# Kernel tuning notes

Measured on AMD Instinct MI355X. Metric: run time of the kernel, lower is better.

## Reference

```python
import jax, jax.numpy as jnp
import numpy as np

HIDDEN_DIM = 2048
NUM_HEADS = 16
HEAD_DIM = HIDDEN_DIM // NUM_HEADS


def setup_inputs() -> dict:
    key = jax.random.key(0)
    ks = jax.random.split(key, 5)
    B, S, D = 1, 2048, HIDDEN_DIM
    scale = 1.0 / np.sqrt(D)
    return {
        "x": jax.random.normal(ks[0], (B, S, D), dtype=jnp.float32),
        "w_q": jax.random.normal(ks[1], (D, D), dtype=jnp.float32) * scale,
        "w_k": jax.random.normal(ks[2], (D, D), dtype=jnp.float32) * scale,
        "w_v": jax.random.normal(ks[3], (D, D), dtype=jnp.float32) * scale,
        "w_o": jax.random.normal(ks[4], (D, D), dtype=jnp.float32) * scale,
    }


def reference(x, w_q, w_k, w_v, w_o):
    # x: (B, S, D). Projections use x @ W.T as in the torch module.
    B, S, D = x.shape
    H, Hd = NUM_HEADS, HEAD_DIM
    q = (x @ w_q.T).reshape(B, S, H, Hd)
    k = (x @ w_k.T).reshape(B, S, H, Hd)
    v = (x @ w_v.T).reshape(B, S, H, Hd)
    scale = 1.0 / np.sqrt(Hd).astype(np.float32)
    # The tiled online-softmax loop computes exact softmax attention.
    scores = jnp.einsum("bqhd,bkhd->bhqk", q, k) * scale  # (B,H,S,S)
    p = jax.nn.softmax(scores, axis=-1)
    o = jnp.einsum("bhqk,bkhd->bqhd", p, v).reshape(B, S, D)
    return o @ w_o.T
```

## Files before the change

kernel.cpp:

```cpp
#include <hip/hip_runtime.h>
#include <hip/hip_bf16.h>
#include <cstdint>
#include <cstddef>

typedef __bf16 bf16x8 __attribute__((ext_vector_type(8)));
typedef float f32x4 __attribute__((ext_vector_type(4)));
typedef unsigned short u16x8 __attribute__((ext_vector_type(8)));
typedef unsigned short u16x4 __attribute__((ext_vector_type(4)));

#define S_LEN 2048
#define DMODEL 2048
#define NHEADS 16
#define HD 128

__device__ inline unsigned short f2bf(float f) {
  union { float f; unsigned int u; } v; v.f = f;
  unsigned int r = (v.u + 0x7fffu + ((v.u >> 16) & 1u)) >> 16;
  return (unsigned short)r;
}

__device__ __forceinline__ void gload16(const unsigned short* g,
                                        unsigned short* lds) {
  __builtin_amdgcn_global_load_lds(
      (const __attribute__((address_space(1))) void*)g,
      (__attribute__((address_space(3))) void*)lds, 16, 0, 0);
}

__global__ void cast_all(const float* __restrict__ x, const float* __restrict__ wq,
                         const float* __restrict__ wk, const float* __restrict__ wv,
                         const float* __restrict__ wo,
                         unsigned short* __restrict__ out, float qscale) {
  const int b = blockIdx.x;
  const int seg = b >> 12;
  const int i = ((b & 4095) * 256 + threadIdx.x) * 4;
  const float* src = seg == 0 ? x : seg == 1 ? wq : seg == 2 ? wk
                   : seg == 3 ? wv : wo;
  const float scale = (seg == 1) ? qscale : 1.0f;
  unsigned short* dst = out + (size_t)seg * ((size_t)S_LEN * DMODEL);
  float4 v = *(const float4*)(src + i);
  u16x4 o;
  o.x = f2bf(v.x * scale); o.y = f2bf(v.y * scale);
  o.z = f2bf(v.z * scale); o.w = f2bf(v.w * scale);
  *(u16x4*)(dst + i) = o;
}

template <int MODE>
__device__ __forceinline__ void gemm_core(
    const unsigned short* __restrict__ A, const unsigned short* __restrict__ B,
    float* __restrict__ Cf, unsigned short* __restrict__ Cb,
    int M, int N, int K, int m0, int n0,
    unsigned short* As, unsigned short* Bs) {
  constexpr int BK = 32;
  const int tid = threadIdx.x;
  const int wave = tid >> 6, lane = tid & 63;
  const int lg = lane >> 4, lr = lane & 15;
  const int rw = (wave >> 1) * 64;
  const int cw = (wave & 1) * 64;

  const int c0 = tid, c1 = tid + 256;
  const unsigned short* Ap0 = A + (size_t)(m0 + (c0 >> 2)) * K + (c0 & 3) * 8;
  const unsigned short* Ap1 = A + (size_t)(m0 + (c1 >> 2)) * K + (c1 & 3) * 8;
  const unsigned short* Bp0 = B + (size_t)(n0 + (c0 >> 2)) * K + (c0 & 3) * 8;
  const unsigned short* Bp1 = B + (size_t)(n0 + (c1 >> 2)) * K + (c1 & 3) * 8;
  unsigned short* as0 = As + wave * 512;
  unsigned short* as1 = As + 2048 + wave * 512;
  unsigned short* bs0 = Bs + wave * 512;
  unsigned short* bs1 = Bs + 2048 + wave * 512;

  f32x4 acc[4][4];
#pragma unroll
  for (int i = 0; i < 4; i++)
#pragma unroll
    for (int j = 0; j < 4; j++) acc[i][j] = (f32x4){0.f, 0.f, 0.f, 0.f};

  const int nk = K / BK;
  for (int kt = 0; kt < nk; ++kt) {
    const int ko = kt * BK;
    __syncthreads();
    gload16(Ap0 + ko, as0);
    gload16(Ap1 + ko, as1);
    gload16(Bp0 + ko, bs0);
    gload16(Bp1 + ko, bs1);
    __syncthreads();

    bf16x8 af[4], bfr[4];
#pragma unroll
    for (int mt = 0; mt < 4; mt++)
      af[mt] = *(const bf16x8*)(As + (rw + mt * 16 + lr) * BK + lg * 8);
#pragma unroll
    for (int nt = 0; nt < 4; nt++)
      bfr[nt] = *(const bf16x8*)(Bs + (cw + nt * 16 + lr) * BK + lg * 8);
#pragma unroll
    for (int mt = 0; mt < 4; mt++)
#pragma unroll
      for (int nt = 0; nt < 4; nt++)
        acc[mt][nt] = __builtin_amdgcn_mfma_f32_16x16x32_bf16(
            af[mt], bfr[nt], acc[mt][nt], 0, 0, 0);
  }

#pragma unroll
  for (int mt = 0; mt < 4; mt++)
#pragma unroll
    for (int nt = 0; nt < 4; nt++) {
      const int col = n0 + cw + nt * 16 + lr;
#pragma unroll
      for (int r = 0; r < 4; r++) {
        const int row = m0 + rw + mt * 16 + lg * 4 + r;
        const float v = acc[mt][nt][r];
        if (MODE == 0) Cf[(size_t)row * N + col] = v;
        else if (MODE == 1) Cb[(size_t)row * N + col] = f2bf(v);
        else Cb[(size_t)col * M + row] = f2bf(v);
      }
    }
}

template <int MODE>
__global__ __launch_bounds__(256, 2) void gemm_bt(
    const unsigned short* __restrict__ A, const unsigned short* __restrict__ B,
    float* __restrict__ Cf, unsigned short* __restrict__ Cb,
    int M, int N, int K) {
  __shared__ unsigned short As[128 * 32];
  __shared__ unsigned short Bs[128 * 32];
  gemm_core<MODE>(A, B, Cf, Cb, M, N, K, blockIdx.y * 128, blockIdx.x * 128,
                  As, Bs);
}

__global__ __launch_bounds__(256, 2) void gemm_qkv(
    const unsigned short* __restrict__ xb, const unsigned short* __restrict__ wqb,
    const unsigned short* __restrict__ wkb, const unsigned short* __restrict__ wvb,
    unsigned short* __restrict__ qb, unsigned short* __restrict__ kb,
    unsigned short* __restrict__ vTb) {
  __shared__ unsigned short As[128 * 32];
  __shared__ unsigned short Bs[128 * 32];
  const int which = blockIdx.x >> 4;
  const int n0 = (blockIdx.x & 15) * 128;
  const int m0 = blockIdx.y * 128;
  if (which == 0)
    gemm_core<1>(xb, wqb, nullptr, qb, S_LEN, DMODEL, DMODEL, m0, n0, As, Bs);
  else if (which == 1)
    gemm_core<1>(xb, wkb, nullptr, kb, S_LEN, DMODEL, DMODEL, m0, n0, As, Bs);
  else
    gemm_core<2>(xb, wvb, nullptr, vTb, S_LEN, DMODEL, DMODEL, m0, n0, As, Bs);
}

__global__ __launch_bounds__(256, 2) void attn_kernel(
    const unsigned short* __restrict__ q, const unsigned short* __restrict__ k,
    const unsigned short* __restrict__ vT, unsigned short* __restrict__ o) {
  constexpr int KT = 64;
  constexpr int KSP = KT + 8;
  __shared__ unsigned short Ks[KT * 136];
  __shared__ unsigned short Vt[HD * KSP];
  __shared__ unsigned short Ps[64 * 64];

  const int tid = threadIdx.x;
  const int w = tid >> 6, lane = tid & 63;
  const int lg = lane >> 4, lr = lane & 15;
  const int h = blockIdx.y;
  const int q0 = blockIdx.x * 64;
  const int qw = q0 + w * 16;

  bf16x8 qf[4];
#pragma unroll
  for (int ks = 0; ks < 4; ks++)
    qf[ks] = *(const bf16x8*)(q + (size_t)(qw + lr) * DMODEL + h * HD +
                              ks * 32 + lg * 8);

  f32x4 Oacc[8];
#pragma unroll
  for (int j = 0; j < 8; j++) Oacc[j] = (f32x4){0.f, 0.f, 0.f, 0.f};
  float lst[4] = {0.f, 0.f, 0.f, 0.f};

  for (int kt = 0; kt < S_LEN / KT; ++kt) {
    __syncthreads();
#pragma unroll
    for (int i = 0; i < 4; i++) {
      const int c = i * 256 + tid;
      const int row = c >> 4, cg = c & 15;
      *(u16x8*)(Ks + row * 136 + cg * 8) =
          *(const u16x8*)(k + (size_t)(kt * KT + row) * DMODEL + h * HD + cg * 8);
    }
#pragma unroll
    for (int i = 0; i < 4; i++) {
      const int c = i * 256 + tid;
      const int row = c >> 3, cg = c & 7;
      *(u16x8*)(Vt + row * KSP + cg * 8) =
          *(const u16x8*)(vT + (size_t)(h * HD + row) * S_LEN + kt * KT + cg * 8);
    }
    __syncthreads();

    f32x4 sc[4];
#pragma unroll
    for (int j = 0; j < 4; j++) sc[j] = (f32x4){0.f, 0.f, 0.f, 0.f};
#pragma unroll
    for (int ks = 0; ks < 4; ks++) {
      bf16x8 kf[4];
#pragma unroll
      for (int nt = 0; nt < 4; nt++)
        kf[nt] = *(const bf16x8*)(Ks + (nt * 16 + lr) * 136 + ks * 32 + lg * 8);
#pragma unroll
      for (int nt = 0; nt < 4; nt++)
        sc[nt] = __builtin_amdgcn_mfma_f32_16x16x32_bf16(qf[ks], kf[nt],
                                                         sc[nt], 0, 0, 0);
    }

#pragma unroll
    for (int r = 0; r < 4; r++) {
      const int rowbase = (w * 16 + lg * 4 + r) * 64;
#pragma unroll
      for (int nt = 0; nt < 4; nt++) {
        const float p = __builtin_amdgcn_exp2f(sc[nt][r]);
        lst[r] += p;
        union { float f; unsigned int u; } cv; cv.f = p;
        Ps[rowbase + ((nt * 16 + lr + lg * 16) & 63)] =
            (unsigned short)(cv.u >> 16);
      }
    }

    const int lrot = ((lr >> 2) & 3) * 16;
#pragma unroll
    for (int ks = 0; ks < 2; ks++) {
      const bf16x8 pf = *(const bf16x8*)(
          Ps + (w * 16 + lr) * 64 + ((ks * 32 + lg * 8 + lrot) & 63));
#pragma unroll
      for (int nt = 0; nt < 8; nt++) {
        const bf16x8 vf =
            *(const bf16x8*)(Vt + (nt * 16 + lr) * KSP + ks * 32 + lg * 8);
        Oacc[nt] = __builtin_amdgcn_mfma_f32_16x16x32_bf16(pf, vf, Oacc[nt],
                                                           0, 0, 0);
      }
    }
  }

#pragma unroll
  for (int r = 0; r < 4; r++) {
    float rs = lst[r];
    rs += __shfl_xor(rs, 1);
    rs += __shfl_xor(rs, 2);
    rs += __shfl_xor(rs, 4);
    rs += __shfl_xor(rs, 8);
    const float inv = 1.0f / rs;
    const int row = qw + lg * 4 + r;
#pragma unroll
    for (int nt = 0; nt < 8; nt++)
      o[(size_t)row * DMODEL + h * HD + nt * 16 + lr] =
          f2bf(Oacc[nt][r] * inv);
  }
}

extern "C" void kernel_launch(void* const* d_in, const int* in_sizes, int n_in,
                              void* d_out, int out_size, void* d_ws, size_t ws_size,
                              hipStream_t stream) {
  (void)in_sizes; (void)n_in; (void)out_size; (void)ws_size;
  const float* x  = (const float*)d_in[0];
  const float* wq = (const float*)d_in[1];
  const float* wk = (const float*)d_in[2];
  const float* wv = (const float*)d_in[3];
  const float* wo = (const float*)d_in[4];
  float* out = (float*)d_out;

  const size_t NE = (size_t)S_LEN * DMODEL;
  unsigned short* ws = (unsigned short*)d_ws;
  unsigned short* xb  = ws + 0 * NE;
  unsigned short* wqb = ws + 1 * NE;
  unsigned short* wkb = ws + 2 * NE;
  unsigned short* wvb = ws + 3 * NE;
  unsigned short* wob = ws + 4 * NE;
  unsigned short* qb  = ws + 5 * NE;
  unsigned short* kb  = ws + 6 * NE;
  unsigned short* vTb = ws + 7 * NE;
  unsigned short* ob  = ws + 8 * NE;

  const float qscale = 0.08838834764831845f * 1.4426950408889634f;

  cast_all<<<dim3(5 * 4096), dim3(256), 0, stream>>>(x, wq, wk, wv, wo, ws,
                                                     qscale);

  gemm_qkv<<<dim3(48, 16), dim3(256), 0, stream>>>(xb, wqb, wkb, wvb, qb, kb,
                                                   vTb);

  attn_kernel<<<dim3(S_LEN / 64, NHEADS), dim3(256), 0, stream>>>(qb, kb, vTb,
                                                                  ob);

  gemm_bt<0><<<dim3(16, 16), dim3(256), 0, stream>>>(ob, wob, out, nullptr,
                                                     S_LEN, DMODEL, DMODEL);
}
```

Before: 282.4 us.

## Prefetch K/V tiles into registers in attention; use 64-row tiles for output GEMM

The attention kernel now loads the next K and V tiles from global memory into registers while the current tile is computed. The idea is to hide global-load latency behind the MFMA and softmax work, at the cost of extra registers and possibly lower occupancy. The output projection moves to a new 64x128-tile GEMM launched with twice as many blocks (512 instead of 256), to fill more CUs on the final GEMM. The fp32 output path is removed from the shared gemm_core.

Result: faster. 271.2 us (-4.0%).

```diff
diff --git a/kernel.cpp b/kernel.cpp
--- a/kernel.cpp
+++ b/kernel.cpp
@@ -47,7 +47,7 @@
 template <int MODE>
 __device__ __forceinline__ void gemm_core(
     const unsigned short* __restrict__ A, const unsigned short* __restrict__ B,
-    float* __restrict__ Cf, unsigned short* __restrict__ Cb,
+    unsigned short* __restrict__ Cb,
     int M, int N, int K, int m0, int n0,
     unsigned short* As, unsigned short* Bs) {
   constexpr int BK = 32;
@@ -107,22 +107,10 @@
       for (int r = 0; r < 4; r++) {
         const int row = m0 + rw + mt * 16 + lg * 4 + r;
         const float v = acc[mt][nt][r];
-        if (MODE == 0) Cf[(size_t)row * N + col] = v;
-        else if (MODE == 1) Cb[(size_t)row * N + col] = f2bf(v);
+        if (MODE == 1) Cb[(size_t)row * N + col] = f2bf(v);
         else Cb[(size_t)col * M + row] = f2bf(v);
       }
     }
-}
-
-template <int MODE>
-__global__ __launch_bounds__(256, 2) void gemm_bt(
-    const unsigned short* __restrict__ A, const unsigned short* __restrict__ B,
-    float* __restrict__ Cf, unsigned short* __restrict__ Cb,
-    int M, int N, int K) {
-  __shared__ unsigned short As[128 * 32];
-  __shared__ unsigned short Bs[128 * 32];
-  gemm_core<MODE>(A, B, Cf, Cb, M, N, K, blockIdx.y * 128, blockIdx.x * 128,
-                  As, Bs);
 }
 
 __global__ __launch_bounds__(256, 2) void gemm_qkv(
@@ -136,11 +124,75 @@
   const int n0 = (blockIdx.x & 15) * 128;
   const int m0 = blockIdx.y * 128;
   if (which == 0)
-    gemm_core<1>(xb, wqb, nullptr, qb, S_LEN, DMODEL, DMODEL, m0, n0, As, Bs);
+    gemm_core<1>(xb, wqb, qb, S_LEN, DMODEL, DMODEL, m0, n0, As, Bs);
   else if (which == 1)
-    gemm_core<1>(xb, wkb, nullptr, kb, S_LEN, DMODEL, DMODEL, m0, n0, As, Bs);
+    gemm_core<1>(xb, wkb, kb, S_LEN, DMODEL, DMODEL, m0, n0, As, Bs);
   else
-    gemm_core<2>(xb, wvb, nullptr, vTb, S_LEN, DMODEL, DMODEL, m0, n0, As, Bs);
+    gemm_core<2>(xb, wvb, vTb, S_LEN, DMODEL, DMODEL, m0, n0, As, Bs);
+}
+
+__global__ __launch_bounds__(256, 2) void gemm_bt64(
+    const unsigned short* __restrict__ A, const unsigned short* __restrict__ B,
+    float* __restrict__ Cf, int M, int N, int K) {
+  constexpr int BK = 32;
+  __shared__ unsigned short As[64 * 32];
+  __shared__ unsigned short Bs[128 * 32];
+  const int tid = threadIdx.x;
+  const int wave = tid >> 6, lane = tid & 63;
+  const int lg = lane >> 4, lr = lane & 15;
+  const int rw = (wave >> 1) * 32;
+  const int cw = (wave & 1) * 64;
+  const int m0 = blockIdx.y * 64, n0 = blockIdx.x * 128;
+
+  const int c0 = tid, c1 = tid + 256;
+  const unsigned short* Ap0 = A + (size_t)(m0 + (c0 >> 2)) * K + (c0 & 3) * 8;
+  const unsigned short* Bp0 = B + (size_t)(n0 + (c0 >> 2)) * K + (c0 & 3) * 8;
+  const unsigned short* Bp1 = B + (size_t)(n0 + (c1 >> 2)) * K + (c1 & 3) * 8;
+  unsigned short* as0 = As + wave * 512;
+  unsigned short* bs0 = Bs + wave * 512;
+  unsigned short* bs1 = Bs + 2048 + wave * 512;
+
+  f32x4 acc[2][4];
+#pragma unroll
+  for (int i = 0; i < 2; i++)
+#pragma unroll
+    for (int j = 0; j < 4; j++) acc[i][j] = (f32x4){0.f, 0.f, 0.f, 0.f};
+
+  const int nk = K / BK;
+  for (int kt = 0; kt < nk; ++kt) {
+    const int ko = kt * BK;
+    __syncthreads();
+    gload16(Ap0 + ko, as0);
+    gload16(Bp0 + ko, bs0);
+    gload16(Bp1 + ko, bs1);
+    __syncthreads();
+
+    bf16x8 af[2], bfr[4];
+#pragma unroll
+    for (int mt = 0; mt < 2; mt++)
+      af[mt] = *(const bf16x8*)(As + (rw + mt * 16 + lr) * BK + lg * 8);
+#pragma unroll
+    for (int nt = 0; nt < 4; nt++)
+      bfr[nt] = *(const bf16x8*)(Bs + (cw + nt * 16 + lr) * BK + lg * 8);
+#pragma unroll
+    for (int mt = 0; mt < 2; mt++)
+#pragma unroll
+      for (int nt = 0; nt < 4; nt++)
+        acc[mt][nt] = __builtin_amdgcn_mfma_f32_16x16x32_bf16(
+            af[mt], bfr[nt], acc[mt][nt], 0, 0, 0);
+  }
+
+#pragma unroll
+  for (int mt = 0; mt < 2; mt++)
+#pragma unroll
+    for (int nt = 0; nt < 4; nt++) {
+      const int col = n0 + cw + nt * 16 + lr;
+#pragma unroll
+      for (int r = 0; r < 4; r++) {
+        const int row = m0 + rw + mt * 16 + lg * 4 + r;
+        Cf[(size_t)row * N + col] = acc[mt][nt][r];
+      }
+    }
 }
 
 __global__ __launch_bounds__(256, 2) void attn_kernel(
@@ -170,23 +222,40 @@
   for (int j = 0; j < 8; j++) Oacc[j] = (f32x4){0.f, 0.f, 0.f, 0.f};
   float lst[4] = {0.f, 0.f, 0.f, 0.f};
 
+  int krow[4], kcg[4], vrow[4], vcg[4];
+#pragma unroll
+  for (int i = 0; i < 4; i++) {
+    const int c = i * 256 + tid;
+    krow[i] = c >> 4; kcg[i] = c & 15;
+    vrow[i] = c >> 3; vcg[i] = c & 7;
+  }
+
+  u16x8 kreg[4], vreg[4];
+#pragma unroll
+  for (int i = 0; i < 4; i++) {
+    kreg[i] = *(const u16x8*)(k + (size_t)(krow[i]) * DMODEL + h * HD + kcg[i] * 8);
+    vreg[i] = *(const u16x8*)(vT + (size_t)(h * HD + vrow[i]) * S_LEN + vcg[i] * 8);
+  }
+
   for (int kt = 0; kt < S_LEN / KT; ++kt) {
     __syncthreads();
 #pragma unroll
     for (int i = 0; i < 4; i++) {
-      const int c = i * 256 + tid;
-      const int row = c >> 4, cg = c & 15;
-      *(u16x8*)(Ks + row * 136 + cg * 8) =
-          *(const u16x8*)(k + (size_t)(kt * KT + row) * DMODEL + h * HD + cg * 8);
-    }
-#pragma unroll
-    for (int i = 0; i < 4; i++) {
-      const int c = i * 256 + tid;
-      const int row = c >> 3, cg = c & 7;
-      *(u16x8*)(Vt + row * KSP + cg * 8) =
-          *(const u16x8*)(vT + (size_t)(h * HD + row) * S_LEN + kt * KT + cg * 8);
-    }
-    __syncthreads();
+      *(u16x8*)(Ks + krow[i] * 136 + kcg[i] * 8) = kreg[i];
+      *(u16x8*)(Vt + vrow[i] * KSP + vcg[i] * 8) = vreg[i];
+    }
+    __syncthreads();
+
+    if (kt + 1 < S_LEN / KT) {
+      const int kbase = (kt + 1) * KT;
+#pragma unroll
+      for (int i = 0; i < 4; i++) {
+        kreg[i] = *(const u16x8*)(k + (size_t)(kbase + krow[i]) * DMODEL +
+                                  h * HD + kcg[i] * 8);
+        vreg[i] = *(const u16x8*)(vT + (size_t)(h * HD + vrow[i]) * S_LEN +
+                                  kbase + vcg[i] * 8);
+      }
+    }
 
     f32x4 sc[4];
 #pragma unroll
@@ -281,6 +350,6 @@
   attn_kernel<<<dim3(S_LEN / 64, NHEADS), dim3(256), 0, stream>>>(qb, kb, vTb,
                                                                   ob);
 
-  gemm_bt<0><<<dim3(16, 16), dim3(256), 0, stream>>>(ob, wob, out, nullptr,
-                                                     S_LEN, DMODEL, DMODEL);
-}
+  gemm_bt64<<<dim3(16, 32), dim3(256), 0, stream>>>(ob, wob, out, S_LEN,
+                                                    DMODEL, DMODEL);
+}
```
